# Optimization experiments

Hardware: AMD Instinct MI355X
Metric: run time of the kernel (lower is better)

The kernel has to match this reference:

```python
import jax, jax.numpy as jnp
import numpy as np

G = 384   # n_gene == input_size
T = 192   # n_timepoint
H = 384   # hidden_size
L = 2     # num_layers


def setup_inputs() -> dict:
    key = jax.random.key(0)
    ks = jax.random.split(key, 8)
    s = 1.0 / np.sqrt(H)  # torch LSTM/Linear default init scale
    x = jax.random.normal(ks[0], (G, T), dtype=jnp.float32)
    # stacked per-layer LSTM params (input_size == hidden_size so layers stack)
    W_ih = jax.random.uniform(ks[1], (L, 4 * H, H), jnp.float32, -s, s)
    W_hh = jax.random.uniform(ks[2], (L, 4 * H, H), jnp.float32, -s, s)
    b_ih = jax.random.uniform(ks[3], (L, 4 * H), jnp.float32, -s, s)
    b_hh = jax.random.uniform(ks[4], (L, 4 * H), jnp.float32, -s, s)
    fc_w = jax.random.uniform(ks[5], (H, 1), jnp.float32, -s, s)
    fc_b = jax.random.uniform(ks[6], (1,), jnp.float32, -s, s)
    return {"x": x, "W_ih": W_ih, "W_hh": W_hh, "b_ih": b_ih,
            "b_hh": b_hh, "fc_w": fc_w, "fc_b": fc_b}


def _run_lstm(seq, W_ih, W_hh, b_ih, b_hh):
    # seq: [T, H_in]; multi-layer unidirectional LSTM, PyTorch gate order i,f,g,o
    for l in range(W_ih.shape[0]):
        wih, whh = W_ih[l], W_hh[l]
        b = b_ih[l] + b_hh[l]

        def step(carry, xt, wih=wih, whh=whh, b=b):
            h, c = carry
            z = xt @ wih.T + h @ whh.T + b  # [4H]
            i, f, g, o = jnp.split(z, 4)
            i = jax.nn.sigmoid(i)
            f = jax.nn.sigmoid(f)
            g = jnp.tanh(g)
            o = jax.nn.sigmoid(o)
            c = f * c + i * g
            h = o * jnp.tanh(c)
            return (h, c), h

        init = (jnp.zeros((whh.shape[-1],), seq.dtype),
                jnp.zeros((whh.shape[-1],), seq.dtype))
        _, seq = jax.lax.scan(step, init, seq)
    return seq  # [T, H]


def reference(x, W_ih, W_hh, b_ih, b_hh, fc_w, fc_b):
    n_gene, n_tp = x.shape
    xt = x.T  # [T, G]
    # masked[i, t, g] = x[g, t] if g == i else 0   (single-gene inputs)
    eye = jnp.eye(n_gene, dtype=x.dtype)
    masked = xt[None, :, :] * eye[:, None, :]        # [G, T, G]
    X_batch = jnp.concatenate([masked, xt[None]], 0)  # [G+1, T, G]

    h_all = jax.vmap(lambda s: _run_lstm(s, W_ih, W_hh, b_ih, b_hh))(X_batch)
    # [G+1, T, H]
    y = (h_all @ fc_w)[..., 0] + fc_b[0]  # [G+1, T]
    yi_pred = y[:n_gene]                  # [G, T] per-gene predictions
    y_all = y[n_gene:n_gene + 1]          # [1, T] all-gene prediction

    attn = jax.nn.softmax(y_all @ yi_pred.T, axis=1)  # [1, G]
    y_pred = (attn @ yi_pred)[0]                       # [T]
    return (y_pred, yi_pred, attn[0])
```

## Files before the change

kernel.cpp:

```cpp
#include <hip/hip_runtime.h>
#include <math.h>

typedef __attribute__((ext_vector_type(8))) short sv8;
typedef __attribute__((ext_vector_type(4))) float fv4;
typedef unsigned short u16;
typedef unsigned int u32;
typedef unsigned long long u64;

#define HD   384
#define NP   1536
#define TDIM 192
#define SEQP 448
#define NBLK 256
#define NPHASE 194

#define OFF_B0HI  0u
#define OFF_B0LO  1179648u
#define OFF_B1AHI 2359296u
#define OFF_B1ALO 3538944u
#define OFF_B1BHI 4718592u
#define OFF_B1BLO 5898240u
#define OFF_WP    7077888u
#define OFF_U     9437184u
#define OFF_B0P   10616832u
#define OFF_B1P   10622976u
#define OFF_H0    10629120u
#define HBUF      688128u
#define OFF_H1    12005376u
#define OFF_ZA    13381632u
#define ZABUF     2752512u
#define OFF_YP    18886656u
#define OFF_YY    27144192u
#define OFF_BAR   27488256u

__device__ __forceinline__ u16 f2bf(float v) {
  unsigned u = __builtin_bit_cast(unsigned, v);
  return (u16)((u + 0x7fffu + ((u >> 16) & 1u)) >> 16);
}
__device__ __forceinline__ float bf2f(u16 s) {
  unsigned u = ((unsigned)s) << 16;
  return __builtin_bit_cast(float, u);
}
__device__ __forceinline__ float sigm(float v) { return 1.0f / (1.0f + expf(-v)); }

__device__ __forceinline__ void store16_sc(float* p, fv4 v) {
  asm volatile("global_store_dwordx4 %0, %1, off sc0 sc1"
               :: "v"(p), "v"(v) : "memory");
}
__device__ __forceinline__ fv4 load16_sc(const float* p) {
  fv4 r;
  asm volatile("global_load_dwordx4 %0, %1, off sc0 sc1"
               : "=v"(r) : "v"(p) : "memory");
  return r;
}


__global__ void pack_weights(const float* __restrict__ W_ih, const float* __restrict__ W_hh,
                             char* __restrict__ wsb) {
  const int idx = blockIdx.x * 256 + threadIdx.x;
  const int NE = 384 * 1536;
  if (idx >= 3 * NE) return;
  const int mat = idx / NE, rem0 = idx % NE;
  const int j = rem0 / 1536, n = rem0 % 1536;
  const int q = n >> 6, rem = n & 63, g = rem >> 4, kl = rem & 15;
  const int hk = q * 16 + kl;
  const int nr = g * 384 + hk;
  float v;
  u16 *dhi, *dlo;
  if (mat == 0) {
    v = W_hh[(size_t)nr * 384 + j];
    dhi = (u16*)(wsb + OFF_B0HI); dlo = (u16*)(wsb + OFF_B0LO);
  } else if (mat == 1) {
    v = W_ih[589824 + (size_t)nr * 384 + j];
    dhi = (u16*)(wsb + OFF_B1AHI); dlo = (u16*)(wsb + OFF_B1ALO);
  } else {
    v = W_hh[589824 + (size_t)nr * 384 + j];
    dhi = (u16*)(wsb + OFF_B1BHI); dlo = (u16*)(wsb + OFF_B1BLO);
  }
  const u16 hi = f2bf(v);
  const u16 lo = f2bf(v - bf2f(hi));
  const size_t off = ((size_t)(j >> 3) * 1536 + n) * 8 + (j & 7);
  dhi[off] = hi; dlo[off] = lo;
}

__global__ void pack_aux(const float* __restrict__ W_ih, const float* __restrict__ b_ih,
                         const float* __restrict__ b_hh, char* __restrict__ wsb) {
  const int idx = blockIdx.x * 256 + threadIdx.x;
  float* Wp = (float*)(wsb + OFF_WP);
  if (idx < 384 * 1536) {
    const int seq = idx / 1536, n = idx % 1536;
    const int q = n >> 6, rem = n & 63, g = rem >> 4, kl = rem & 15;
    const int hk = q * 16 + kl;
    Wp[idx] = W_ih[(size_t)(g * 384 + hk) * 384 + seq];
  }
  if (idx < 1536) {
    const int q = idx >> 6, rem = idx & 63, g = rem >> 4, kl = rem & 15;
    const int nr = g * 384 + (q * 16 + kl);
    ((float*)(wsb + OFF_B0P))[idx] = b_ih[nr] + b_hh[nr];
    ((float*)(wsb + OFF_B1P))[idx] = b_ih[1536 + nr] + b_hh[1536 + nr];
  }
}

__global__ __launch_bounds__(256) void compute_U(const float* __restrict__ x,
                                                 char* __restrict__ wsb) {
  const float* Wp = (const float*)(wsb + OFF_WP);
  float* U = (float*)(wsb + OFF_U);
  __shared__ float xs[384];
  const int t = blockIdx.x;
  for (int j = threadIdx.x; j < 384; j += 256) xs[j] = x[(size_t)j * TDIM + t];
  __syncthreads();
  for (int n = threadIdx.x; n < 1536; n += 256) {
    float a = 0.0f;
    for (int j = 0; j < 384; ++j) a = fmaf(xs[j], Wp[(size_t)j * NP + n], a);
    U[(size_t)t * NP + n] = a;
  }
}


__device__ __forceinline__ void load_a(sv8 ah[12], sv8 al[12], const u32* __restrict__ plane,
                                       int rowA, int lkc) {
  const u32* base = plane + (size_t)rowA * HD + lkc * 8;
  #pragma unroll
  for (int kc = 0; kc < 12; ++kc) {
    const u64* p = (const u64*)(base + kc * 32);
    u64 q0 = __hip_atomic_load(p + 0, __ATOMIC_RELAXED, __HIP_MEMORY_SCOPE_SYSTEM);
    u64 q1 = __hip_atomic_load(p + 1, __ATOMIC_RELAXED, __HIP_MEMORY_SCOPE_SYSTEM);
    u64 q2 = __hip_atomic_load(p + 2, __ATOMIC_RELAXED, __HIP_MEMORY_SCOPE_SYSTEM);
    u64 q3 = __hip_atomic_load(p + 3, __ATOMIC_RELAXED, __HIP_MEMORY_SCOPE_SYSTEM);
    const u32 w0 = (u32)q0, w1 = (u32)(q0 >> 32), w2 = (u32)q1, w3 = (u32)(q1 >> 32);
    const u32 w4 = (u32)q2, w5 = (u32)(q2 >> 32), w6 = (u32)q3, w7 = (u32)(q3 >> 32);
    union { sv8 v; u32 w[4]; } H, L;
    H.w[0] = __builtin_amdgcn_perm(w1, w0, 0x05040100u);
    H.w[1] = __builtin_amdgcn_perm(w3, w2, 0x05040100u);
    H.w[2] = __builtin_amdgcn_perm(w5, w4, 0x05040100u);
    H.w[3] = __builtin_amdgcn_perm(w7, w6, 0x05040100u);
    L.w[0] = __builtin_amdgcn_perm(w1, w0, 0x07060302u);
    L.w[1] = __builtin_amdgcn_perm(w3, w2, 0x07060302u);
    L.w[2] = __builtin_amdgcn_perm(w5, w4, 0x07060302u);
    L.w[3] = __builtin_amdgcn_perm(w7, w6, 0x07060302u);
    ah[kc] = H.v; al[kc] = L.v;
  }
}

__device__ __forceinline__ void gemm384(fv4 acc[4], const sv8 ah[12], const sv8 al[12],
                                        const u16* __restrict__ Bhi, const u16* __restrict__ Blo,
                                        int n0, int lrow, int lkc) {
  const size_t bb = ((size_t)lkc * NP + n0 + lrow) * 8;
  #pragma unroll 4
  for (int kc = 0; kc < 12; ++kc) {
    const size_t bo = bb + (size_t)kc * 4 * NP * 8;
    #pragma unroll
    for (int g = 0; g < 4; ++g) {
      const sv8 bh = *(const sv8*)(Bhi + bo + g * 16 * 8);
      const sv8 bl = *(const sv8*)(Blo + bo + g * 16 * 8);
      acc[g] = __builtin_amdgcn_mfma_f32_16x16x32_bf16(ah[kc], bh, acc[g], 0, 0, 0);
      acc[g] = __builtin_amdgcn_mfma_f32_16x16x32_bf16(ah[kc], bl, acc[g], 0, 0, 0);
      acc[g] = __builtin_amdgcn_mfma_f32_16x16x32_bf16(al[kc], bh, acc[g], 0, 0, 0);
    }
  }
}

__global__ __launch_bounds__(256, 1) void lstm_coop(const float* __restrict__ x,
                                                    const float* __restrict__ fc_w,
                                                    char* __restrict__ wsb) {
  const u16* B0hi  = (const u16*)(wsb + OFF_B0HI);
  const u16* B0lo  = (const u16*)(wsb + OFF_B0LO);
  const u16* B1ahi = (const u16*)(wsb + OFF_B1AHI);
  const u16* B1alo = (const u16*)(wsb + OFF_B1ALO);
  const u16* B1bhi = (const u16*)(wsb + OFF_B1BHI);
  const u16* B1blo = (const u16*)(wsb + OFF_B1BLO);
  const float* Wp  = (const float*)(wsb + OFF_WP);
  const float* U   = (const float*)(wsb + OFF_U);
  const float* b0p = (const float*)(wsb + OFF_B0P);
  const float* b1p = (const float*)(wsb + OFF_B1P);
  float* Yp = (float*)(wsb + OFF_YP);
  u32* arr  = (u32*)(wsb + OFF_BAR);

  const int tid = threadIdx.x;
  const int lane = tid & 63, wv = tid >> 6;
  const int lrow = lane & 15, lkc = lane >> 4;
  const int bid = blockIdx.x;
  const int xcd = bid & 7, ib = bid >> 3;

  int s_type[2], s_kg[2], s_mt[2];
  bool s_ok[2];
  float bias4[2][4], fcw2[2], wp16[2][16];
  float cst[2][4] = {{0.f,0.f,0.f,0.f},{0.f,0.f,0.f,0.f}};
  #pragma unroll
  for (int s = 0; s < 2; ++s) {
    const int jx = ib * 2 + s;
    s_ok[s] = (jx < 63);
    const int kgl = jx < 63 ? jx / 21 : 0;
    const int rem = jx < 63 ? jx % 21 : 0;
    s_type[s] = rem / 7; s_mt[s] = rem % 7; s_kg[s] = xcd * 3 + kgl;
    const int n0 = s_kg[s] * 64;
    const float* bp = (s_type[s] == 0) ? b0p : b1p;
    #pragma unroll
    for (int g = 0; g < 4; ++g) bias4[s][g] = bp[n0 + g * 16 + lrow];
    fcw2[s] = fc_w[s_kg[s] * 16 + lrow];
    #pragma unroll
    for (int r = 0; r < 4; ++r) {
      const int seq = s_mt[s] * 64 + wv * 16 + lkc * 4 + r;
      #pragma unroll
      for (int g = 0; g < 4; ++g)
        wp16[s][r * 4 + g] = (s_type[s] == 0 && seq < 384)
                               ? Wp[(size_t)seq * NP + n0 + g * 16 + lrow] : 0.0f;
    }
  }

  for (int p = 0; p < NPHASE; ++p) {
    const u32* h0R = (const u32*)(wsb + OFF_H0 + (size_t)((p + 1) & 1) * HBUF);
    u32*       h0W = (u32*)(wsb + OFF_H0 + (size_t)(p & 1) * HBUF);
    const u32* h1R = (const u32*)(wsb + OFF_H1 + (size_t)((p + 1) & 1) * HBUF);
    u32*       h1W = (u32*)(wsb + OFF_H1 + (size_t)(p & 1) * HBUF);
    float*       zaW = (float*)(wsb + OFF_ZA + (size_t)((p + 1) & 1) * ZABUF);
    const float* zaR = (const float*)(wsb + OFF_ZA + (size_t)(p & 1) * ZABUF);

    #pragma unroll
    for (int s = 0; s < 2; ++s) {
      if (!s_ok[s]) continue;
      const int ty = s_type[s], kg = s_kg[s], mt = s_mt[s];
      const int n0 = kg * 64, seq0 = mt * 64 + wv * 16, ke = kg * 16 + lrow;
      sv8 ah[12], al[12];
      fv4 acc[4] = {{0.f,0.f,0.f,0.f},{0.f,0.f,0.f,0.f},{0.f,0.f,0.f,0.f},{0.f,0.f,0.f,0.f}};
      if (ty == 0) {
        if (p > 191) continue;
        const int t = p;
        load_a(ah, al, h0R, seq0 + lrow, lkc);
        gemm384(acc, ah, al, B0hi, B0lo, n0, lrow, lkc);
        #pragma unroll
        for (int r = 0; r < 4; ++r) {
          const int seq = seq0 + lkc * 4 + r;
          float zi = acc[0][r] + bias4[s][0], zf = acc[1][r] + bias4[s][1],
                zg = acc[2][r] + bias4[s][2], zo = acc[3][r] + bias4[s][3];
          if (seq < 384) {
            const float xv = x[(size_t)seq * TDIM + t];
            zi = fmaf(xv, wp16[s][r * 4 + 0], zi);
            zf = fmaf(xv, wp16[s][r * 4 + 1], zf);
            zg = fmaf(xv, wp16[s][r * 4 + 2], zg);
            zo = fmaf(xv, wp16[s][r * 4 + 3], zo);
          } else if (seq == 384) {
            const float* ur = U + (size_t)t * NP + n0;
            zi += ur[lrow]; zf += ur[16 + lrow]; zg += ur[32 + lrow]; zo += ur[48 + lrow];
          }
          const float ig = sigm(zi), fg = sigm(zf), gv = tanhf(zg), og = sigm(zo);
          const float cn = fg * cst[s][r] + ig * gv;
          cst[s][r] = cn;
          const float h = og * tanhf(cn);
          const u16 hh = f2bf(h); const u16 hl = f2bf(h - bf2f(hh));
          __hip_atomic_store(h0W + (size_t)seq * HD + ke, (u32)hh | ((u32)hl << 16),
                             __ATOMIC_RELAXED, __HIP_MEMORY_SCOPE_SYSTEM);
        }
      } else if (ty == 1) {
        if (p < 1 || p > 192) continue;
        load_a(ah, al, h0R, seq0 + lrow, lkc);
        gemm384(acc, ah, al, B1ahi, B1alo, n0, lrow, lkc);
        float* zb = zaW + (((size_t)kg * 7 + mt) * 4 + wv) * 1024;
        #pragma unroll
        for (int g = 0; g < 4; ++g) {
          fv4 zc;
          #pragma unroll
          for (int r = 0; r < 4; ++r) zc[r] = acc[g][r] + bias4[s][g];
          store16_sc(zb + g * 256 + lane * 4, zc);
        }
      } else {
        if (p < 2) continue;
        const int t = p - 2;
        load_a(ah, al, h1R, seq0 + lrow, lkc);
        gemm384(acc, ah, al, B1bhi, B1blo, n0, lrow, lkc);
        const float* zb = zaR + (((size_t)kg * 7 + mt) * 4 + wv) * 1024;
        fv4 zv4[4];
        zv4[0] = load16_sc(zb + 0 * 256 + lane * 4);
        zv4[1] = load16_sc(zb + 1 * 256 + lane * 4);
        zv4[2] = load16_sc(zb + 2 * 256 + lane * 4);
        zv4[3] = load16_sc(zb + 3 * 256 + lane * 4);
        asm volatile("s_waitcnt vmcnt(0)" ::: "memory");
        __builtin_amdgcn_sched_barrier(0);
        #pragma unroll
        for (int r = 0; r < 4; ++r) {
          const int seq = seq0 + lkc * 4 + r;
          const float zi = acc[0][r] + zv4[0][r], zf = acc[1][r] + zv4[1][r],
                      zg = acc[2][r] + zv4[2][r], zo = acc[3][r] + zv4[3][r];
          const float ig = sigm(zi), fg = sigm(zf), gv = tanhf(zg), og = sigm(zo);
          const float cn = fg * cst[s][r] + ig * gv;
          cst[s][r] = cn;
          const float h = og * tanhf(cn);
          const u16 hh = f2bf(h); const u16 hl = f2bf(h - bf2f(hh));
          __hip_atomic_store(h1W + (size_t)seq * HD + ke, (u32)hh | ((u32)hl << 16),
                             __ATOMIC_RELAXED, __HIP_MEMORY_SCOPE_SYSTEM);
          float yv = h * fcw2[s];
          yv += __shfl_xor(yv, 1); yv += __shfl_xor(yv, 2);
          yv += __shfl_xor(yv, 4); yv += __shfl_xor(yv, 8);
          if (lrow == 0) Yp[((size_t)t * SEQP + seq) * 24 + kg] = yv;
        }
      }
    }
    __syncthreads();
    if (tid == 0)
      __hip_atomic_store(&arr[(size_t)bid * 16], (u32)(p + 1),
                         __ATOMIC_RELAXED, __HIP_MEMORY_SCOPE_SYSTEM);
    {
      const u32 tgt = (u32)(p + 1);
      while (__hip_atomic_load(&arr[(size_t)tid * 16],
                               __ATOMIC_RELAXED, __HIP_MEMORY_SCOPE_SYSTEM) < tgt)
        __builtin_amdgcn_s_sleep(2);
    }
    __syncthreads();
  }
}


__global__ void y_final(const float* __restrict__ fc_b, char* __restrict__ wsb) {
  const float* Yp = (const float*)(wsb + OFF_YP);
  float* Y = (float*)(wsb + OFF_YY);
  const int t = blockIdx.x;
  const int seq = threadIdx.x;
  if (seq < 385) {
    const float* p = Yp + ((size_t)t * SEQP + seq) * 24;
    float s = fc_b[0];
    #pragma unroll
    for (int k = 0; k < 24; ++k) s += p[k];
    Y[(size_t)seq * TDIM + t] = s;
  }
}

__global__ void copy_yi(char* __restrict__ wsb, float* __restrict__ out) {
  const float* Y = (const float*)(wsb + OFF_YY);
  const int i = blockIdx.x * 256 + threadIdx.x;
  if (i < 384 * 192) out[192 + i] = Y[i];
}

__global__ __launch_bounds__(384) void attn_final(char* __restrict__ wsb,
                                                  float* __restrict__ out) {
  const float* Y = (const float*)(wsb + OFF_YY);
  __shared__ float sc[384];
  __shared__ float redm[8], reds[8];
  const int j = threadIdx.x;
  const float* ya = Y + (size_t)384 * TDIM;
  float dot = 0.f;
  for (int t = 0; t < TDIM; ++t) dot = fmaf(ya[t], Y[(size_t)j * TDIM + t], dot);
  float m = dot;
  m = fmaxf(m, __shfl_xor(m, 32)); m = fmaxf(m, __shfl_xor(m, 16));
  m = fmaxf(m, __shfl_xor(m, 8));  m = fmaxf(m, __shfl_xor(m, 4));
  m = fmaxf(m, __shfl_xor(m, 2));  m = fmaxf(m, __shfl_xor(m, 1));
  if ((j & 63) == 0) redm[j >> 6] = m;
  __syncthreads();
  float M = redm[0];
  #pragma unroll
  for (int w = 1; w < 6; ++w) M = fmaxf(M, redm[w]);
  const float e = expf(dot - M);
  float ss = e;
  ss += __shfl_xor(ss, 32); ss += __shfl_xor(ss, 16); ss += __shfl_xor(ss, 8);
  ss += __shfl_xor(ss, 4);  ss += __shfl_xor(ss, 2);  ss += __shfl_xor(ss, 1);
  if ((j & 63) == 0) reds[j >> 6] = ss;
  __syncthreads();
  float S = 0.f;
  #pragma unroll
  for (int w = 0; w < 6; ++w) S += reds[w];
  const float a = e / S;
  sc[j] = a;
  out[192 + 73728 + j] = a;
  __syncthreads();
  if (j < 192) {
    float acc = 0.f;
    for (int jj = 0; jj < 384; ++jj) acc = fmaf(sc[jj], Y[(size_t)jj * TDIM + j], acc);
    out[j] = acc;
  }
}

extern "C" void kernel_launch(void* const* d_in, const int* in_sizes, int n_in,
                              void* d_out, int out_size, void* d_ws, size_t ws_size,
                              hipStream_t stream) {
  const float* x    = (const float*)d_in[0];
  const float* W_ih = (const float*)d_in[1];
  const float* W_hh = (const float*)d_in[2];
  const float* b_ih = (const float*)d_in[3];
  const float* b_hh = (const float*)d_in[4];
  const float* fc_w = (const float*)d_in[5];
  const float* fc_b = (const float*)d_in[6];
  float* out = (float*)d_out;
  char* wsb  = (char*)d_ws;

  hipMemsetAsync(wsb + OFF_H0, 0, 2 * HBUF * 2, stream);
  hipMemsetAsync(wsb + OFF_BAR, 0, 16384, stream);
  hipLaunchKernelGGL(pack_weights, dim3(6912), dim3(256), 0, stream, W_ih, W_hh, wsb);
  hipLaunchKernelGGL(pack_aux,     dim3(2304), dim3(256), 0, stream, W_ih, b_ih, b_hh, wsb);
  hipLaunchKernelGGL(compute_U,    dim3(192),  dim3(256), 0, stream, x, wsb);

  void* args[] = {(void*)&x, (void*)&fc_w, (void*)&wsb};
  hipLaunchCooperativeKernel((void*)lstm_coop, dim3(NBLK), dim3(256), args, 0, stream);

  hipLaunchKernelGGL(y_final,  dim3(192), dim3(448), 0, stream, fc_b, wsb);
  hipLaunchKernelGGL(copy_yi,  dim3(288), dim3(256), 0, stream, wsb, out);
  hipLaunchKernelGGL(attn_final, dim3(1), dim3(384), 0, stream, wsb, out);
}
```

Baseline: 8.497 ms.

## Fuse all three LSTM gate tasks per block and keep layer-1 input preactivations in registers

Each block now owns one (kg, mt) tile and runs the layer-0 recurrence, the layer-1 input GEMM and the layer-1 recurrence itself. The layer-1 input preactivation is carried in registers across phases, so the global za buffer with its store/load round trip goes away. The grid drops from 256 to 168 blocks, which shortens the barrier poll. Hidden states are transposed through LDS so they leave as one 16-byte store instead of many scalar atomic stores. Each block now does three 384-deep GEMMs serially per phase, which lengthens the per-phase critical path and raises register pressure.

After: 12.29 ms. 44.6% more time.

```diff
diff --git a/kernel.cpp b/kernel.cpp
--- a/kernel.cpp
+++ b/kernel.cpp
@@ -3,6 +3,7 @@
 
 typedef __attribute__((ext_vector_type(8))) short sv8;
 typedef __attribute__((ext_vector_type(4))) float fv4;
+typedef __attribute__((ext_vector_type(4))) unsigned int uv4;
 typedef unsigned short u16;
 typedef unsigned int u32;
 typedef unsigned long long u64;
@@ -11,7 +12,7 @@
 #define NP   1536
 #define TDIM 192
 #define SEQP 448
-#define NBLK 256
+#define NBLK 168
 #define NPHASE 194
 
 #define OFF_B0HI  0u
@@ -27,8 +28,6 @@
 #define OFF_H0    10629120u
 #define HBUF      688128u
 #define OFF_H1    12005376u
-#define OFF_ZA    13381632u
-#define ZABUF     2752512u
 #define OFF_YP    18886656u
 #define OFF_YY    27144192u
 #define OFF_BAR   27488256u
@@ -46,12 +45,6 @@
 __device__ __forceinline__ void store16_sc(float* p, fv4 v) {
   asm volatile("global_store_dwordx4 %0, %1, off sc0 sc1"
                :: "v"(p), "v"(v) : "memory");
-}
-__device__ __forceinline__ fv4 load16_sc(const float* p) {
-  fv4 r;
-  asm volatile("global_load_dwordx4 %0, %1, off sc0 sc1"
-               : "=v"(r) : "v"(p) : "memory");
-  return r;
 }
 
 
@@ -181,131 +174,138 @@
   const int lrow = lane & 15, lkc = lane >> 4;
   const int bid = blockIdx.x;
   const int xcd = bid & 7, ib = bid >> 3;
-
-  int s_type[2], s_kg[2], s_mt[2];
-  bool s_ok[2];
-  float bias4[2][4], fcw2[2], wp16[2][16];
-  float cst[2][4] = {{0.f,0.f,0.f,0.f},{0.f,0.f,0.f,0.f}};
-  #pragma unroll
-  for (int s = 0; s < 2; ++s) {
-    const int jx = ib * 2 + s;
-    s_ok[s] = (jx < 63);
-    const int kgl = jx < 63 ? jx / 21 : 0;
-    const int rem = jx < 63 ? jx % 21 : 0;
-    s_type[s] = rem / 7; s_mt[s] = rem % 7; s_kg[s] = xcd * 3 + kgl;
-    const int n0 = s_kg[s] * 64;
-    const float* bp = (s_type[s] == 0) ? b0p : b1p;
+  const int kgl = ib / 7, mt = ib % 7;
+  const int kg = xcd * 3 + kgl;
+  const int n0 = kg * 64, ke = kg * 16 + lrow;
+  const int seq0 = mt * 64 + wv * 16;
+
+  __shared__ u32 xpose[4][16][16];
+
+  float b0v[4], b1v[4], wp16[16];
+  float cst0[4] = {0.f, 0.f, 0.f, 0.f};
+  float cst1[4] = {0.f, 0.f, 0.f, 0.f};
+  fv4 zaPrev[4], zaNew[4];
+  #pragma unroll
+  for (int g = 0; g < 4; ++g) {
+    b0v[g] = b0p[n0 + g * 16 + lrow];
+    b1v[g] = b1p[n0 + g * 16 + lrow];
+    zaPrev[g] = fv4{0.f, 0.f, 0.f, 0.f};
+    zaNew[g]  = fv4{0.f, 0.f, 0.f, 0.f};
+  }
+  const float fcwv = fc_w[ke];
+  #pragma unroll
+  for (int r = 0; r < 4; ++r) {
+    const int seq = seq0 + lkc * 4 + r;
     #pragma unroll
-    for (int g = 0; g < 4; ++g) bias4[s][g] = bp[n0 + g * 16 + lrow];
-    fcw2[s] = fc_w[s_kg[s] * 16 + lrow];
-    #pragma unroll
-    for (int r = 0; r < 4; ++r) {
-      const int seq = s_mt[s] * 64 + wv * 16 + lkc * 4 + r;
-      #pragma unroll
-      for (int g = 0; g < 4; ++g)
-        wp16[s][r * 4 + g] = (s_type[s] == 0 && seq < 384)
-                               ? Wp[(size_t)seq * NP + n0 + g * 16 + lrow] : 0.0f;
-    }
-  }
+    for (int g = 0; g < 4; ++g)
+      wp16[r * 4 + g] = (seq < 384) ? Wp[(size_t)seq * NP + n0 + g * 16 + lrow] : 0.0f;
+  }
+
+  const int xs = lane & 15, xc = lane >> 4;
 
   for (int p = 0; p < NPHASE; ++p) {
     const u32* h0R = (const u32*)(wsb + OFF_H0 + (size_t)((p + 1) & 1) * HBUF);
     u32*       h0W = (u32*)(wsb + OFF_H0 + (size_t)(p & 1) * HBUF);
     const u32* h1R = (const u32*)(wsb + OFF_H1 + (size_t)((p + 1) & 1) * HBUF);
     u32*       h1W = (u32*)(wsb + OFF_H1 + (size_t)(p & 1) * HBUF);
-    float*       zaW = (float*)(wsb + OFF_ZA + (size_t)((p + 1) & 1) * ZABUF);
-    const float* zaR = (const float*)(wsb + OFF_ZA + (size_t)(p & 1) * ZABUF);
+
+    sv8 ah0[12], al0[12], ah1[12], al1[12];
+    if (p <= 192) load_a(ah0, al0, h0R, seq0 + lrow, lkc);
+    if (p >= 2)   load_a(ah1, al1, h1R, seq0 + lrow, lkc);
+
+    if (p <= 191) {
+      const int t = p;
+      fv4 acc[4] = {{0.f,0.f,0.f,0.f},{0.f,0.f,0.f,0.f},{0.f,0.f,0.f,0.f},{0.f,0.f,0.f,0.f}};
+      gemm384(acc, ah0, al0, B0hi, B0lo, n0, lrow, lkc);
+      u32 hv[4];
+      #pragma unroll
+      for (int r = 0; r < 4; ++r) {
+        const int seq = seq0 + lkc * 4 + r;
+        float zi = acc[0][r] + b0v[0], zf = acc[1][r] + b0v[1],
+              zg = acc[2][r] + b0v[2], zo = acc[3][r] + b0v[3];
+        if (seq < 384) {
+          const float xv = x[(size_t)seq * TDIM + t];
+          zi = fmaf(xv, wp16[r * 4 + 0], zi);
+          zf = fmaf(xv, wp16[r * 4 + 1], zf);
+          zg = fmaf(xv, wp16[r * 4 + 2], zg);
+          zo = fmaf(xv, wp16[r * 4 + 3], zo);
+        } else if (seq == 384) {
+          const float* ur = U + (size_t)t * NP + n0;
+          zi += ur[lrow]; zf += ur[16 + lrow]; zg += ur[32 + lrow]; zo += ur[48 + lrow];
+        }
+        const float ig = sigm(zi), fg = sigm(zf), gv = tanhf(zg), og = sigm(zo);
+        const float cn = fg * cst0[r] + ig * gv;
+        cst0[r] = cn;
+        const float h = og * tanhf(cn);
+        const u16 hh = f2bf(h); const u16 hl = f2bf(h - bf2f(hh));
+        hv[r] = (u32)hh | ((u32)hl << 16);
+      }
+      #pragma unroll
+      for (int r = 0; r < 4; ++r) xpose[wv][lkc * 4 + r][lrow] = hv[r];
+      {
+        const uv4 uv = *(const uv4*)&xpose[wv][xs][xc * 4];
+        store16_sc((float*)(h0W + (size_t)(seq0 + xs) * HD + kg * 16 + xc * 4),
+                   __builtin_bit_cast(fv4, uv));
+      }
+    }
+
+    if (p >= 1 && p <= 192) {
+      fv4 acc[4] = {{0.f,0.f,0.f,0.f},{0.f,0.f,0.f,0.f},{0.f,0.f,0.f,0.f},{0.f,0.f,0.f,0.f}};
+      gemm384(acc, ah0, al0, B1ahi, B1alo, n0, lrow, lkc);
+      #pragma unroll
+      for (int g = 0; g < 4; ++g) {
+        #pragma unroll
+        for (int r = 0; r < 4; ++r) zaNew[g][r] = acc[g][r] + b1v[g];
+      }
+    }
+
+    if (p >= 2) {
+      const int t = p - 2;
+      fv4 acc[4] = {{0.f,0.f,0.f,0.f},{0.f,0.f,0.f,0.f},{0.f,0.f,0.f,0.f},{0.f,0.f,0.f,0.f}};
+      gemm384(acc, ah1, al1, B1bhi, B1blo, n0, lrow, lkc);
+      u32 hv[4];
+      #pragma unroll
+      for (int r = 0; r < 4; ++r) {
+        const int seq = seq0 + lkc * 4 + r;
+        const float zi = acc[0][r] + zaPrev[0][r];
+        const float zf = acc[1][r] + zaPrev[1][r];
+        const float zg = acc[2][r] + zaPrev[2][r];
+        const float zo = acc[3][r] + zaPrev[3][r];
+        const float ig = sigm(zi), fg = sigm(zf), gv = tanhf(zg), og = sigm(zo);
+        const float cn = fg * cst1[r] + ig * gv;
+        cst1[r] = cn;
+        const float h = og * tanhf(cn);
+        const u16 hh = f2bf(h); const u16 hl = f2bf(h - bf2f(hh));
+        hv[r] = (u32)hh | ((u32)hl << 16);
+        float yv = h * fcwv;
+        yv += __shfl_xor(yv, 1); yv += __shfl_xor(yv, 2);
+        yv += __shfl_xor(yv, 4); yv += __shfl_xor(yv, 8);
+        if (lrow == 0) Yp[((size_t)t * SEQP + seq) * 24 + kg] = yv;
+      }
+      #pragma unroll
+      for (int r = 0; r < 4; ++r) xpose[wv][lkc * 4 + r][lrow] = hv[r];
+      {
+        const uv4 uv = *(const uv4*)&xpose[wv][xs][xc * 4];
+        store16_sc((float*)(h1W + (size_t)(seq0 + xs) * HD + kg * 16 + xc * 4),
+                   __builtin_bit_cast(fv4, uv));
+      }
+    }
 
     #pragma unroll
-    for (int s = 0; s < 2; ++s) {
-      if (!s_ok[s]) continue;
-      const int ty = s_type[s], kg = s_kg[s], mt = s_mt[s];
-      const int n0 = kg * 64, seq0 = mt * 64 + wv * 16, ke = kg * 16 + lrow;
-      sv8 ah[12], al[12];
-      fv4 acc[4] = {{0.f,0.f,0.f,0.f},{0.f,0.f,0.f,0.f},{0.f,0.f,0.f,0.f},{0.f,0.f,0.f,0.f}};
-      if (ty == 0) {
-        if (p > 191) continue;
-        const int t = p;
-        load_a(ah, al, h0R, seq0 + lrow, lkc);
-        gemm384(acc, ah, al, B0hi, B0lo, n0, lrow, lkc);
-        #pragma unroll
-        for (int r = 0; r < 4; ++r) {
-          const int seq = seq0 + lkc * 4 + r;
-          float zi = acc[0][r] + bias4[s][0], zf = acc[1][r] + bias4[s][1],
-                zg = acc[2][r] + bias4[s][2], zo = acc[3][r] + bias4[s][3];
-          if (seq < 384) {
-            const float xv = x[(size_t)seq * TDIM + t];
-            zi = fmaf(xv, wp16[s][r * 4 + 0], zi);
-            zf = fmaf(xv, wp16[s][r * 4 + 1], zf);
-            zg = fmaf(xv, wp16[s][r * 4 + 2], zg);
-            zo = fmaf(xv, wp16[s][r * 4 + 3], zo);
-          } else if (seq == 384) {
-            const float* ur = U + (size_t)t * NP + n0;
-            zi += ur[lrow]; zf += ur[16 + lrow]; zg += ur[32 + lrow]; zo += ur[48 + lrow];
-          }
-          const float ig = sigm(zi), fg = sigm(zf), gv = tanhf(zg), og = sigm(zo);
-          const float cn = fg * cst[s][r] + ig * gv;
-          cst[s][r] = cn;
-          const float h = og * tanhf(cn);
-          const u16 hh = f2bf(h); const u16 hl = f2bf(h - bf2f(hh));
-          __hip_atomic_store(h0W + (size_t)seq * HD + ke, (u32)hh | ((u32)hl << 16),
-                             __ATOMIC_RELAXED, __HIP_MEMORY_SCOPE_SYSTEM);
-        }
-      } else if (ty == 1) {
-        if (p < 1 || p > 192) continue;
-        load_a(ah, al, h0R, seq0 + lrow, lkc);
-        gemm384(acc, ah, al, B1ahi, B1alo, n0, lrow, lkc);
-        float* zb = zaW + (((size_t)kg * 7 + mt) * 4 + wv) * 1024;
-        #pragma unroll
-        for (int g = 0; g < 4; ++g) {
-          fv4 zc;
-          #pragma unroll
-          for (int r = 0; r < 4; ++r) zc[r] = acc[g][r] + bias4[s][g];
-          store16_sc(zb + g * 256 + lane * 4, zc);
-        }
-      } else {
-        if (p < 2) continue;
-        const int t = p - 2;
-        load_a(ah, al, h1R, seq0 + lrow, lkc);
-        gemm384(acc, ah, al, B1bhi, B1blo, n0, lrow, lkc);
-        const float* zb = zaR + (((size_t)kg * 7 + mt) * 4 + wv) * 1024;
-        fv4 zv4[4];
-        zv4[0] = load16_sc(zb + 0 * 256 + lane * 4);
-        zv4[1] = load16_sc(zb + 1 * 256 + lane * 4);
-        zv4[2] = load16_sc(zb + 2 * 256 + lane * 4);
-        zv4[3] = load16_sc(zb + 3 * 256 + lane * 4);
-        asm volatile("s_waitcnt vmcnt(0)" ::: "memory");
-        __builtin_amdgcn_sched_barrier(0);
-        #pragma unroll
-        for (int r = 0; r < 4; ++r) {
-          const int seq = seq0 + lkc * 4 + r;
-          const float zi = acc[0][r] + zv4[0][r], zf = acc[1][r] + zv4[1][r],
-                      zg = acc[2][r] + zv4[2][r], zo = acc[3][r] + zv4[3][r];
-          const float ig = sigm(zi), fg = sigm(zf), gv = tanhf(zg), og = sigm(zo);
-          const float cn = fg * cst[s][r] + ig * gv;
-          cst[s][r] = cn;
-          const float h = og * tanhf(cn);
-          const u16 hh = f2bf(h); const u16 hl = f2bf(h - bf2f(hh));
-          __hip_atomic_store(h1W + (size_t)seq * HD + ke, (u32)hh | ((u32)hl << 16),
-                             __ATOMIC_RELAXED, __HIP_MEMORY_SCOPE_SYSTEM);
-          float yv = h * fcw2[s];
-          yv += __shfl_xor(yv, 1); yv += __shfl_xor(yv, 2);
-          yv += __shfl_xor(yv, 4); yv += __shfl_xor(yv, 8);
-          if (lrow == 0) Yp[((size_t)t * SEQP + seq) * 24 + kg] = yv;
-        }
-      }
-    }
+    for (int g = 0; g < 4; ++g) zaPrev[g] = zaNew[g];
+
+    asm volatile("s_waitcnt vmcnt(0)" ::: "memory");
     __syncthreads();
     if (tid == 0)
       __hip_atomic_store(&arr[(size_t)bid * 16], (u32)(p + 1),
                          __ATOMIC_RELAXED, __HIP_MEMORY_SCOPE_SYSTEM);
-    {
-      const u32 tgt = (u32)(p + 1);
+    if (tid < NBLK) {
       while (__hip_atomic_load(&arr[(size_t)tid * 16],
-                               __ATOMIC_RELAXED, __HIP_MEMORY_SCOPE_SYSTEM) < tgt)
+                               __ATOMIC_RELAXED, __HIP_MEMORY_SCOPE_SYSTEM) < (u32)(p + 1))
         __builtin_amdgcn_s_sleep(2);
     }
     __syncthreads();
+    __builtin_amdgcn_sched_barrier(0);
   }
 }
 
```
